# Performance work log

Measured on AMD Instinct MI355X. Metric: run time of the kernel, lower is better.

Reference implementation:

```python
import jax, jax.numpy as jnp
import numpy as np

N = 100000          # num_node
E = 3200000         # num_edge (avg degree 32)
IN_CH = 128
HID = 64
NUM_REL = 8
HIST_SIZE = 1024


def setup_inputs() -> dict:
    key = jax.random.key(0)
    k = jax.random.split(key, 8)
    x = jax.random.normal(k[0], (N, IN_CH), jnp.float32)
    # glorot-uniform per original reset_parameters()
    limit = np.sqrt(6.0 / (IN_CH + HID)).astype(np.float32)
    rel_weight = jax.random.uniform(k[1], (NUM_REL, IN_CH, HID), jnp.float32,
                                    minval=-limit, maxval=limit)
    history_buffer = jax.random.normal(k[2], (N, HID), jnp.float32)
    # uniform-degree CSR: every node has E//N incident edges
    deg = E // N
    ptr = (jnp.arange(N + 1, dtype=jnp.int32) * deg)
    idx = jax.random.randint(k[3], (E,), 0, N, jnp.int32)          # src nodes
    edge_types = jax.random.randint(k[4], (E,), 0, NUM_REL, jnp.int32)
    count = jnp.zeros((NUM_REL,), jnp.int32)  # recomputed inside fwd; ignored
    hit = jax.random.bernoulli(k[5], 0.1, (N,))
    history_map = jnp.where(hit,
                            jax.random.randint(k[6], (N,), 0, HIST_SIZE, jnp.int32),
                            jnp.int32(-1))
    used_mask = jax.random.bernoulli(k[7], 0.95, (N,))
    return {
        "x": x, "rel_weight": rel_weight, "history_buffer": history_buffer,
        "ptr": ptr, "idx": idx, "edge_types": edge_types, "count": count,
        "history_map": history_map, "used_mask": used_mask,
        "history_size": HIST_SIZE, "num_node": N,
    }


def reference(x, rel_weight, history_buffer, ptr, idx, edge_types, count,
              history_map, used_mask, history_size, num_node):
    num_rel = rel_weight.shape[0]
    num_edge = idx.shape[0]            # static; == ptr[num_node] by construction
    deg = ptr[1:num_node + 1] - ptr[:num_node]                     # [N]
    dst = jnp.repeat(jnp.arange(num_node, dtype=jnp.int32), deg,
                     total_repeat_length=num_edge)                 # [E]
    src = idx
    # rel[~used_mask[src]] = num_rel  -> those edges contribute nothing
    rel = jnp.where(used_mask[src], edge_types, jnp.int32(num_rel))
    valid = rel < num_rel
    relc = jnp.minimum(rel, num_rel - 1)
    # RGCNOP: out[dst] += x[src] @ W[rel].  Precompute x @ W for all relations
    # ([N, R, HID], cheap GEMM) then do the irregular gather + segment-sum.
    xW = jnp.einsum('ni,rio->nro', x, rel_weight)                  # [N,R,HID]
    msg = xW[src, relc] * valid[:, None].astype(x.dtype)           # [E,HID]
    out = jax.ops.segment_sum(msg, dst, num_segments=num_node)     # [N,HID]
    out = out / deg[:, None].astype(x.dtype)                       # degree norm
    if history_size > 0:
        out = jnp.where((history_map != -1)[:, None], history_buffer, out)
    return out  # original returns (out, his) with his aliasing out
```

## Files before the change

kernel.cpp:

```cpp
#include <hip/hip_runtime.h>
#include <stdint.h>

#define IN_CH 128
#define HID   64
#define NREL  8

typedef __attribute__((ext_vector_type(8))) short bf16x8;
typedef __attribute__((ext_vector_type(4))) float f32x4;
typedef __attribute__((ext_vector_type(2))) float f32x2;

__device__ __forceinline__ unsigned short f2bf(float f) {
  union { float f; unsigned u; } v; v.f = f;
  unsigned r = v.u + 0x7fffu + ((v.u >> 16) & 1u);
  return (unsigned short)(r >> 16);
}

__global__ __launch_bounds__(256) void k_prep(const float* __restrict__ W,
                                              const unsigned char* __restrict__ um,
                                              unsigned short* __restrict__ Wt,
                                              int* __restrict__ flag, int total) {
  int t = blockIdx.x * 256 + threadIdx.x;
  if (t < total) {
    int r = t >> 13;
    int rem = t & 8191;
    int o = rem >> 7;
    int k = rem & 127;
    Wt[t] = f2bf(W[(r << 13) + k * HID + o]);
  }
  if (blockIdx.x == 0 && threadIdx.x < 64) {
    unsigned w = ((const unsigned*)um)[threadIdx.x];
    int s = (int)((w & 0xffu) + ((w >> 8) & 0xffu) + ((w >> 16) & 0xffu) + ((w >> 24) & 0xffu));
#pragma unroll
    for (int m = 1; m < 64; m <<= 1) s += __shfl_xor(s, m);
    if (threadIdx.x == 0) *flag = (s > 150) ? 1 : 0;
  }
}

__global__ __launch_bounds__(512) void k_gemm(const float* __restrict__ x,
                                              const unsigned short* __restrict__ Wt,
                                              unsigned char* __restrict__ xW,
                                              const void* __restrict__ um,
                                              const int* __restrict__ flagp,
                                              int ntiles, int N) {
  __shared__ unsigned short lds[2][16 * IN_CH];
  int w    = threadIdx.x >> 6;
  int lane = threadIdx.x & 63;
  int l15  = lane & 15;
  int kg   = lane >> 4;

  bf16x8 wf[16];
  {
    const unsigned short* wb = Wt + ((size_t)(w * HID + l15)) * IN_CH + kg * 8;
#pragma unroll
    for (int ot = 0; ot < 4; ++ot)
#pragma unroll
      for (int ki = 0; ki < 4; ++ki)
        wf[ot * 4 + ki] = *(const bf16x8*)(wb + (ot * 16) * IN_CH + ki * 32);
  }

  int bytes = *flagp;
  const unsigned char* um8 = (const unsigned char*)um;
  const int* um32 = (const int*)um;

  int node_s = threadIdx.x >> 5;
  int q      = threadIdx.x & 31;
  int wboff  = node_s * 256 + ((q * 8) ^ ((node_s & 7) << 4));
  int rswz   = (l15 & 7) << 4;

  int stride = gridDim.x;
  int t = blockIdx.x;
  if (t >= ntiles) return;

  float4 pre; float mpre;
  {
    int n = t * 16 + node_s;
    int nc = n < N ? n : N - 1;
    pre = *(const float4*)(x + (size_t)nc * IN_CH + q * 4);
    mpre = (bytes ? (int)um8[nc] : um32[nc]) != 0 ? 1.0f : 0.0f;
    ushort4 b;
    b.x = f2bf(pre.x * mpre); b.y = f2bf(pre.y * mpre);
    b.z = f2bf(pre.z * mpre); b.w = f2bf(pre.w * mpre);
    *(ushort4*)((char*)(&lds[0][0]) + wboff) = b;
  }

  int buf = 0;
  for (; t < ntiles; t += stride) {
    int tn = t + stride;
    bool has_next = tn < ntiles;
    if (has_next) {
      int n = tn * 16 + node_s;
      int nc = n < N ? n : N - 1;
      pre = *(const float4*)(x + (size_t)nc * IN_CH + q * 4);
      mpre = (bytes ? (int)um8[nc] : um32[nc]) != 0 ? 1.0f : 0.0f;
    }
    __syncthreads();
    bf16x8 xf[4];
    const char* lbase = (const char*)(&lds[buf][0]);
#pragma unroll
    for (int ki = 0; ki < 4; ++ki) {
      int c = (kg * 16 + ki * 64) ^ rswz;
      xf[ki] = *(const bf16x8*)(lbase + l15 * 256 + c);
    }
    int node = t * 16 + l15;
    bool st = node < N;
    size_t orow = (size_t)node * (NREL * HID) + w * HID + kg * 4;
#pragma unroll
    for (int ot = 0; ot < 4; ++ot) {
      f32x4 acc = {0.f, 0.f, 0.f, 0.f};
#pragma unroll
      for (int ki = 0; ki < 4; ++ki)
        acc = __builtin_amdgcn_mfma_f32_16x16x32_bf16(wf[ot * 4 + ki], xf[ki], acc, 0, 0, 0);
      if (st) {
        int p = __builtin_amdgcn_cvt_pk_fp8_f32(acc[0], acc[1], 0, false);
        p = __builtin_amdgcn_cvt_pk_fp8_f32(acc[2], acc[3], p, true);
        *(unsigned*)(xW + orow + ot * 16) = (unsigned)p;
      }
    }
    if (has_next) {
      ushort4 b;
      b.x = f2bf(pre.x * mpre); b.y = f2bf(pre.y * mpre);
      b.z = f2bf(pre.z * mpre); b.w = f2bf(pre.w * mpre);
      *(ushort4*)((char*)(&lds[buf ^ 1][0]) + wboff) = b;
    }
    buf ^= 1;
  }
}

__global__ __launch_bounds__(256) void k_agg(const unsigned char* __restrict__ xW,
                                             const int* __restrict__ ptr,
                                             const int* __restrict__ idx,
                                             const int* __restrict__ et,
                                             const int* __restrict__ hmap,
                                             const float* __restrict__ hbuf,
                                             const int* __restrict__ hszp,
                                             float* __restrict__ out, int N) {
  int wid = (int)((blockIdx.x * 256u + threadIdx.x) >> 6);
  if (wid >= N) return;
  int lane = threadIdx.x & 63;
  int g = lane >> 3, c8 = lane & 7;
  size_t orow = (size_t)wid * HID + (size_t)c8 * 8;

  int hs = *hszp;
  int hm = hmap[wid];
  if (hs > 0 && hm != -1) {
    if (g == 0) {
      float4 h0 = *(const float4*)(hbuf + orow);
      float4 h1 = *(const float4*)(hbuf + orow + 4);
      *(float4*)(out + orow) = h0;
      *(float4*)(out + orow + 4) = h1;
    }
    return;
  }

  int e0 = ptr[wid], e1 = ptr[wid + 1];

  float a[8] = {0.f, 0.f, 0.f, 0.f, 0.f, 0.f, 0.f, 0.f};
  for (int base = e0; base < e1; base += 32) {
    int src[4], rel[4];
    float ok[4];
#pragma unroll
    for (int j = 0; j < 4; ++j) {
      int e = base + g + j * 8;
      bool v = e < e1;
      int ee = v ? e : e0;
      src[j] = idx[ee];
      rel[j] = et[ee];
      ok[j] = v ? 1.0f : 0.0f;
    }
    uint2 vv[4];
#pragma unroll
    for (int j = 0; j < 4; ++j) {
      int rc = rel[j] & (NREL - 1);
      vv[j] = *(const uint2*)(xW + (size_t)src[j] * (NREL * HID) + rc * HID + c8 * 8);
    }
#pragma unroll
    for (int j = 0; j < 4; ++j) {
      f32x2 p0 = __builtin_amdgcn_cvt_pk_f32_fp8((int)vv[j].x, false);
      f32x2 p1 = __builtin_amdgcn_cvt_pk_f32_fp8((int)vv[j].x, true);
      f32x2 p2 = __builtin_amdgcn_cvt_pk_f32_fp8((int)vv[j].y, false);
      f32x2 p3 = __builtin_amdgcn_cvt_pk_f32_fp8((int)vv[j].y, true);
      a[0] += ok[j] * p0[0]; a[1] += ok[j] * p0[1];
      a[2] += ok[j] * p1[0]; a[3] += ok[j] * p1[1];
      a[4] += ok[j] * p2[0]; a[5] += ok[j] * p2[1];
      a[6] += ok[j] * p3[0]; a[7] += ok[j] * p3[1];
    }
  }
#pragma unroll
  for (int m = 8; m < 64; m <<= 1) {
#pragma unroll
    for (int c = 0; c < 8; ++c) a[c] += __shfl_xor(a[c], m);
  }
  if (g == 0) {
    int deg = e1 - e0;
    float inv = deg > 0 ? 1.0f / (float)deg : 0.0f;
    float4 o0, o1;
    o0.x = a[0] * inv; o0.y = a[1] * inv; o0.z = a[2] * inv; o0.w = a[3] * inv;
    o1.x = a[4] * inv; o1.y = a[5] * inv; o1.z = a[6] * inv; o1.w = a[7] * inv;
    *(float4*)(out + orow) = o0;
    *(float4*)(out + orow + 4) = o1;
  }
}

extern "C" void kernel_launch(void* const* d_in, const int* in_sizes, int n_in,
                              void* d_out, int out_size, void* d_ws, size_t ws_size,
                              hipStream_t stream) {
  const float* x  = (const float*)d_in[0];
  const float* W  = (const float*)d_in[1];
  const float* hb = (const float*)d_in[2];
  const int* ptr  = (const int*)d_in[3];
  const int* idx  = (const int*)d_in[4];
  const int* et   = (const int*)d_in[5];
  const int* hmap = (const int*)d_in[7];
  const void* um  = d_in[8];
  const int* hsz  = (const int*)d_in[9];
  int N = in_sizes[3] - 1;
  float* out = (float*)d_out;

  unsigned short* Wt = (unsigned short*)d_ws;
  int* flag = (int*)((char*)d_ws + 131072);
  unsigned char* xW = (unsigned char*)d_ws + (1 << 20);

  int totW = NREL * IN_CH * HID;
  k_prep<<<(totW + 255) / 256, 256, 0, stream>>>(W, (const unsigned char*)um, Wt, flag, totW);

  int ntiles = (N + 15) / 16;
  int gblocks = ntiles < 1024 ? ntiles : 1024;
  k_gemm<<<gblocks, 512, 0, stream>>>(x, Wt, xW, um, flag, ntiles, N);

  long long athreads = (long long)N * 64;
  k_agg<<<(int)((athreads + 255) / 256), 256, 0, stream>>>(xW, ptr, idx, et, hmap, hb,
                                                           hsz, out, N);
}
```

Before: 234.8 us.

## Permute GEMM weight rows so each lane stores 16 contiguous fp8 outputs

The weight prep now permutes output-channel order so that the MFMA accumulator fragments for the four output tiles map to 16 contiguous fp8 bytes per lane. Each lane can then write one 16-byte store instead of four scattered 4-byte stores. The GEMM kernel also processes 64 nodes per step (four 16-node sub-tiles) with a larger LDS double buffer and fewer blocks, to amortise synchronisation and prefetch overhead. The trade-offs are more registers for the four prefetched rows and a larger LDS footprint, which may lower occupancy.

After: 213.5 us. -9.1%, faster.

```diff
diff --git a/kernel.cpp b/kernel.cpp
--- a/kernel.cpp
+++ b/kernel.cpp
@@ -22,10 +22,10 @@
   int t = blockIdx.x * 256 + threadIdx.x;
   if (t < total) {
     int r = t >> 13;
-    int rem = t & 8191;
-    int o = rem >> 7;
-    int k = rem & 127;
-    Wt[t] = f2bf(W[(r << 13) + k * HID + o]);
+    int p = (t >> 7) & 63;
+    int k = t & 127;
+    int o = (((p >> 2) & 3) << 4) + (((p >> 4) & 3) << 2) + (p & 3);
+    Wt[t] = f2bf(W[(r << 13) + (k << 6) + o]);
   }
   if (blockIdx.x == 0 && threadIdx.x < 64) {
     unsigned w = ((const unsigned*)um)[threadIdx.x];
@@ -41,8 +41,8 @@
                                               unsigned char* __restrict__ xW,
                                               const void* __restrict__ um,
                                               const int* __restrict__ flagp,
-                                              int ntiles, int N) {
-  __shared__ unsigned short lds[2][16 * IN_CH];
+                                              int nsteps, int N) {
+  __shared__ unsigned short lds[2][64 * IN_CH];
   int w    = threadIdx.x >> 6;
   int lane = threadIdx.x & 63;
   int l15  = lane & 15;
@@ -69,58 +69,71 @@
 
   int stride = gridDim.x;
   int t = blockIdx.x;
-  if (t >= ntiles) return;
-
-  float4 pre; float mpre;
-  {
-    int n = t * 16 + node_s;
+  if (t >= nsteps) return;
+
+  float4 pre[4]; float mpre[4];
+#pragma unroll
+  for (int j = 0; j < 4; ++j) {
+    int n = t * 64 + node_s + j * 16;
     int nc = n < N ? n : N - 1;
-    pre = *(const float4*)(x + (size_t)nc * IN_CH + q * 4);
-    mpre = (bytes ? (int)um8[nc] : um32[nc]) != 0 ? 1.0f : 0.0f;
+    pre[j] = *(const float4*)(x + (size_t)nc * IN_CH + q * 4);
+    mpre[j] = (bytes ? (int)um8[nc] : um32[nc]) != 0 ? 1.0f : 0.0f;
+  }
+#pragma unroll
+  for (int j = 0; j < 4; ++j) {
     ushort4 b;
-    b.x = f2bf(pre.x * mpre); b.y = f2bf(pre.y * mpre);
-    b.z = f2bf(pre.z * mpre); b.w = f2bf(pre.w * mpre);
-    *(ushort4*)((char*)(&lds[0][0]) + wboff) = b;
+    b.x = f2bf(pre[j].x * mpre[j]); b.y = f2bf(pre[j].y * mpre[j]);
+    b.z = f2bf(pre[j].z * mpre[j]); b.w = f2bf(pre[j].w * mpre[j]);
+    *(ushort4*)((char*)(&lds[0][0]) + wboff + j * 4096) = b;
   }
 
   int buf = 0;
-  for (; t < ntiles; t += stride) {
+  for (; t < nsteps; t += stride) {
     int tn = t + stride;
-    bool has_next = tn < ntiles;
+    bool has_next = tn < nsteps;
     if (has_next) {
-      int n = tn * 16 + node_s;
-      int nc = n < N ? n : N - 1;
-      pre = *(const float4*)(x + (size_t)nc * IN_CH + q * 4);
-      mpre = (bytes ? (int)um8[nc] : um32[nc]) != 0 ? 1.0f : 0.0f;
+#pragma unroll
+      for (int j = 0; j < 4; ++j) {
+        int n = tn * 64 + node_s + j * 16;
+        int nc = n < N ? n : N - 1;
+        pre[j] = *(const float4*)(x + (size_t)nc * IN_CH + q * 4);
+        mpre[j] = (bytes ? (int)um8[nc] : um32[nc]) != 0 ? 1.0f : 0.0f;
+      }
     }
     __syncthreads();
-    bf16x8 xf[4];
-    const char* lbase = (const char*)(&lds[buf][0]);
-#pragma unroll
-    for (int ki = 0; ki < 4; ++ki) {
-      int c = (kg * 16 + ki * 64) ^ rswz;
-      xf[ki] = *(const bf16x8*)(lbase + l15 * 256 + c);
-    }
-    int node = t * 16 + l15;
-    bool st = node < N;
-    size_t orow = (size_t)node * (NREL * HID) + w * HID + kg * 4;
-#pragma unroll
-    for (int ot = 0; ot < 4; ++ot) {
-      f32x4 acc = {0.f, 0.f, 0.f, 0.f};
+#pragma unroll
+    for (int s = 0; s < 4; ++s) {
+      const char* lbase = (const char*)(&lds[buf][0]) + s * 4096;
+      bf16x8 xf[4];
 #pragma unroll
       for (int ki = 0; ki < 4; ++ki)
-        acc = __builtin_amdgcn_mfma_f32_16x16x32_bf16(wf[ot * 4 + ki], xf[ki], acc, 0, 0, 0);
-      if (st) {
+        xf[ki] = *(const bf16x8*)(lbase + l15 * 256 + ((kg * 16 + ki * 64) ^ rswz));
+      int node = t * 64 + s * 16 + l15;
+      bool st = node < N;
+      unsigned pdw[4];
+#pragma unroll
+      for (int ot = 0; ot < 4; ++ot) {
+        f32x4 acc = {0.f, 0.f, 0.f, 0.f};
+#pragma unroll
+        for (int ki = 0; ki < 4; ++ki)
+          acc = __builtin_amdgcn_mfma_f32_16x16x32_bf16(wf[ot * 4 + ki], xf[ki], acc, 0, 0, 0);
         int p = __builtin_amdgcn_cvt_pk_fp8_f32(acc[0], acc[1], 0, false);
         p = __builtin_amdgcn_cvt_pk_fp8_f32(acc[2], acc[3], p, true);
-        *(unsigned*)(xW + orow + ot * 16) = (unsigned)p;
+        pdw[ot] = (unsigned)p;
+      }
+      if (st) {
+        uint4 v; v.x = pdw[0]; v.y = pdw[1]; v.z = pdw[2]; v.w = pdw[3];
+        *(uint4*)(xW + (size_t)node * (NREL * HID) + w * HID + kg * 16) = v;
       }
     }
     if (has_next) {
-      ushort4 b;
-      b.x = f2bf(pre.x * mpre); b.y = f2bf(pre.y * mpre);
-      b.z = f2bf(pre.z * mpre); b.w = f2bf(pre.w * mpre);
-      *(ushort4*)((char*)(&lds[buf ^ 1][0]) + wboff) = b;
+#pragma unroll
+      for (int j = 0; j < 4; ++j) {
+        ushort4 b;
+        b.x = f2bf(pre[j].x * mpre[j]); b.y = f2bf(pre[j].y * mpre[j]);
+        b.z = f2bf(pre[j].z * mpre[j]); b.w = f2bf(pre[j].w * mpre[j]);
+        *(ushort4*)((char*)(&lds[buf ^ 1][0]) + wboff + j * 4096) = b;
+      }
     }
     buf ^= 1;
   }
@@ -223,9 +236,9 @@
   int totW = NREL * IN_CH * HID;
   k_prep<<<(totW + 255) / 256, 256, 0, stream>>>(W, (const unsigned char*)um, Wt, flag, totW);
 
-  int ntiles = (N + 15) / 16;
-  int gblocks = ntiles < 1024 ? ntiles : 1024;
-  k_gemm<<<gblocks, 512, 0, stream>>>(x, Wt, xW, um, flag, ntiles, N);
+  int nsteps = (N + 63) / 64;
+  int gblocks = nsteps < 512 ? nsteps : 512;
+  k_gemm<<<gblocks, 512, 0, stream>>>(x, Wt, xW, um, flag, nsteps, N);
 
   long long athreads = (long long)N * 64;
   k_agg<<<(int)((athreads + 255) / 256), 256, 0, stream>>>(xW, ptr, idx, et, hmap, hb,
```
